# Performance work log

Measured on AMD Instinct MI355X. Metric: run time of the kernel, lower is better.

The kernel has to match this reference:

```python
import jax, jax.numpy as jnp
import numpy as np
import math

B, N, K, DV = 4, 8192, 32, 256
HID = 64


def _linear_params(key, n_in, n_out):
    # torch nn.Linear default init: U(-1/sqrt(n_in), 1/sqrt(n_in))
    kw, kb = jax.random.split(key)
    bound = 1.0 / math.sqrt(n_in)
    W = jax.random.uniform(kw, (n_out, n_in), jnp.float32, -bound, bound)
    b = jax.random.uniform(kb, (n_out,), jnp.float32, -bound, bound)
    return W, b


def setup_inputs() -> dict:
    key = jax.random.key(0)
    ks = jax.random.split(key, 9)
    q = jax.random.normal(ks[0], (B, N, 1, 3), jnp.float32)
    k = jax.random.normal(ks[1], (B, N, K, 3), jnp.float32)
    v = jax.random.normal(ks[2], (B, N, K, DV), jnp.float32)
    q_w0, q_b0 = _linear_params(ks[3], 3, HID)
    q_w1, q_b1 = _linear_params(ks[4], HID, HID)
    q_w2, q_b2 = _linear_params(ks[5], HID, HID)
    k_w0, k_b0 = _linear_params(ks[6], 3, HID)
    k_w1, k_b1 = _linear_params(ks[7], HID, HID)
    k_w2, k_b2 = _linear_params(ks[8], HID, HID)
    return {"q": q, "k": k, "v": v,
            "q_w0": q_w0, "q_b0": q_b0, "q_w1": q_w1, "q_b1": q_b1,
            "q_w2": q_w2, "q_b2": q_b2,
            "k_w0": k_w0, "k_b0": k_b0, "k_w1": k_w1, "k_b1": k_b1,
            "k_w2": k_w2, "k_b2": k_b2}


def _mlp(x, w0, b0, w1, b1, w2, b2):
    # 3-layer MLP: ReLU on first two layers, last layer linear
    x = jax.nn.relu(x @ w0.T + b0)
    x = jax.nn.relu(x @ w1.T + b1)
    return x @ w2.T + b2


def reference(q, k, v, q_w0, q_b0, q_w1, q_b1, q_w2, q_b2,
              k_w0, k_b0, k_w1, k_b1, k_w2, k_b2):
    # NOTE: scale uses the PRE-MLP last dim of q (=3), matching the torch code
    scale = 1.0 / math.sqrt(q.shape[-1])
    qe = _mlp(q, q_w0, q_b0, q_w1, q_b1, q_w2, q_b2)  # [B,N,1,64]
    ke = _mlp(k, k_w0, k_b0, k_w1, k_b1, k_w2, k_b2)  # [B,N,K,64]
    weight = jnp.einsum('bnqd,bnkd->bnqk', qe, ke) * scale  # [B,N,1,K]
    weight = jax.nn.softmax(weight, axis=-1)
    weight = jnp.squeeze(weight, -2)[..., None]             # [B,N,K,1]
    out = (weight * v).sum(-2)                              # [B,N,DV]
    return out
```

## Files before the change

kernel.cpp:

```cpp
#include <hip/hip_runtime.h>
#include <hip/hip_bf16.h>

typedef __attribute__((ext_vector_type(8))) short bf16x8;
typedef __attribute__((ext_vector_type(4))) float f32x4;

union BF8U { unsigned u[4]; bf16x8 v; };

#define PF 8

__device__ __forceinline__ unsigned f2bf1(float x){
  unsigned u = __builtin_bit_cast(unsigned, x);
  return (u + 0x7FFFu + ((u >> 16) & 1u)) >> 16;
}
__device__ __forceinline__ unsigned packbf(float a, float b){
  return f2bf1(a) | (f2bf1(b) << 16);
}
__device__ __forceinline__ unsigned cvt2(float a, float b){
  return (unsigned)__bfloat16_as_ushort(__float2bfloat16(a))
       | ((unsigned)__bfloat16_as_ushort(__float2bfloat16(b)) << 16);
}

__device__ __forceinline__ int act_addr(int r, int byteInRow){
  return r*128 + (byteInRow ^ ((r & 7) << 4));
}
#define LDS_SZ 16384

__global__ __launch_bounds__(256) void prep_kernel(
    const float* __restrict__ kw0, const float* __restrict__ kb0,
    const float* __restrict__ kw1, const float* __restrict__ kw2,
    const float* __restrict__ qw0, const float* __restrict__ qb0,
    const float* __restrict__ qw1, const float* __restrict__ qw2,
    unsigned* __restrict__ WF)
{
  const int t = threadIdx.x;
  const int path = blockIdx.x;
  const float* w0 = path ? qw0 : kw0;
  const float* b0 = path ? qb0 : kb0;
  const float* w1 = path ? qw1 : kw1;
  const float* w2 = path ? qw2 : kw2;
  unsigned* out = WF + path * 5120;
#pragma unroll
  for (int u = 0; u < 4; ++u) {
    int s2 = t + 256*u;
    int j2 = s2 & 3, l = (s2 >> 2) & 63, ct = s2 >> 8;
    int feat = 16*ct + (l & 15);
    int k0 = 8*(l >> 4) + 2*j2;
    float a = (k0   < 3) ? w0[feat*3 + k0]   : (k0   == 3 ? b0[feat] : 0.f);
    float b = (k0+1 < 3) ? w0[feat*3 + k0+1] : (k0+1 == 3 ? b0[feat] : 0.f);
    out[s2] = packbf(a, b);
  }
#pragma unroll
  for (int u = 0; u < 8; ++u) {
    int s2 = t + 256*u;
    int j2 = s2 & 3, l = (s2 >> 2) & 63, ctks = s2 >> 8;
    int feat = 16*(ctks & 3) + (l & 15);
    int k = 32*(ctks >> 2) + 8*(l >> 4) + 2*j2;
    out[1024 + s2] = packbf(w1[feat*64 + k], w1[feat*64 + k + 1]);
    out[3072 + s2] = packbf(w2[feat*64 + k], w2[feat*64 + k + 1]);
  }
}

__device__ __forceinline__ void mlp3(char* lds, int t,
    const float xv[2][3],
    const unsigned* __restrict__ WF,
    const float* __restrict__ b1, const float* __restrict__ b2,
    f32x4 acc2[4][2])
{
  const int lane = t & 63;
  const int q = lane >> 4, lm = lane & 15;
  const int wbase = (t >> 6) * 32;

  bf16x8 a0[2];
#pragma unroll
  for (int rt = 0; rt < 2; ++rt) {
    BF8U u;
    u.u[0] = (q == 0) ? cvt2(xv[rt][0], xv[rt][1]) : 0u;
    u.u[1] = (q == 0) ? cvt2(xv[rt][2], 1.0f)      : 0u;
    u.u[2] = 0u; u.u[3] = 0u;
    a0[rt] = u.v;
  }

  f32x4 h[4][2];

  {
    bf16x8 wf[4];
#pragma unroll
    for (int ft = 0; ft < 4; ++ft)
      wf[ft] = *(const bf16x8*)(WF + ft*256 + lane*4);
#pragma unroll
    for (int ft = 0; ft < 4; ++ft)
#pragma unroll
      for (int rt = 0; rt < 2; ++rt) {
        h[ft][rt] = (f32x4)(0.f);
        h[ft][rt] = __builtin_amdgcn_mfma_f32_16x16x32_bf16(wf[ft], a0[rt], h[ft][rt], 0, 0, 0);
      }
#pragma unroll
    for (int ft = 0; ft < 4; ++ft)
#pragma unroll
      for (int rt = 0; rt < 2; ++rt) {
        int rr = wbase + 16*rt + lm;
        f32x4 vv = h[ft][rt];
        uint2 wp;
        wp.x = cvt2(fmaxf(vv[0],0.f), fmaxf(vv[1],0.f));
        wp.y = cvt2(fmaxf(vv[2],0.f), fmaxf(vv[3],0.f));
        *(uint2*)(lds + act_addr(rr, (16*ft + 4*q)*2)) = wp;
      }
  }

  {
    bf16x8 a1[2][2];
#pragma unroll
    for (int rt = 0; rt < 2; ++rt)
#pragma unroll
      for (int ks = 0; ks < 2; ++ks)
        a1[rt][ks] = *(const bf16x8*)(lds + act_addr(wbase + 16*rt + lm, 64*ks + 16*q));
    bf16x8 wf[8];
#pragma unroll
    for (int c = 0; c < 8; ++c)
      wf[c] = *(const bf16x8*)(WF + 1024 + c*256 + lane*4);
#pragma unroll
    for (int ft = 0; ft < 4; ++ft)
#pragma unroll
      for (int rt = 0; rt < 2; ++rt) {
        h[ft][rt] = (f32x4)(0.f);
        h[ft][rt] = __builtin_amdgcn_mfma_f32_16x16x32_bf16(wf[ft],   a1[rt][0], h[ft][rt], 0, 0, 0);
        h[ft][rt] = __builtin_amdgcn_mfma_f32_16x16x32_bf16(wf[4+ft], a1[rt][1], h[ft][rt], 0, 0, 0);
      }
#pragma unroll
    for (int ft = 0; ft < 4; ++ft) {
      f32x4 b1f = *(const f32x4*)(b1 + 16*ft + 4*q);
#pragma unroll
      for (int rt = 0; rt < 2; ++rt) {
        int rr = wbase + 16*rt + lm;
        f32x4 vv = h[ft][rt];
        uint2 wp;
        wp.x = cvt2(fmaxf(vv[0]+b1f[0],0.f), fmaxf(vv[1]+b1f[1],0.f));
        wp.y = cvt2(fmaxf(vv[2]+b1f[2],0.f), fmaxf(vv[3]+b1f[3],0.f));
        *(uint2*)(lds + act_addr(rr, (16*ft + 4*q)*2)) = wp;
      }
    }
  }

  {
    bf16x8 a2[2][2];
#pragma unroll
    for (int rt = 0; rt < 2; ++rt)
#pragma unroll
      for (int ks = 0; ks < 2; ++ks)
        a2[rt][ks] = *(const bf16x8*)(lds + act_addr(wbase + 16*rt + lm, 64*ks + 16*q));
    bf16x8 wf[8];
#pragma unroll
    for (int c = 0; c < 8; ++c)
      wf[c] = *(const bf16x8*)(WF + 3072 + c*256 + lane*4);
#pragma unroll
    for (int ft = 0; ft < 4; ++ft)
#pragma unroll
      for (int rt = 0; rt < 2; ++rt) {
        acc2[ft][rt] = (f32x4)(0.f);
        acc2[ft][rt] = __builtin_amdgcn_mfma_f32_16x16x32_bf16(wf[ft],   a2[rt][0], acc2[ft][rt], 0, 0, 0);
        acc2[ft][rt] = __builtin_amdgcn_mfma_f32_16x16x32_bf16(wf[4+ft], a2[rt][1], acc2[ft][rt], 0, 0, 0);
      }
#pragma unroll
    for (int ft = 0; ft < 4; ++ft) {
      f32x4 b2f = *(const f32x4*)(b2 + 16*ft + 4*q);
#pragma unroll
      for (int rt = 0; rt < 2; ++rt)
#pragma unroll
        for (int i = 0; i < 4; ++i) acc2[ft][rt][i] += b2f[i];
    }
  }
}

__global__ __launch_bounds__(256, 3) void qe_mfma_kernel(
    const float* __restrict__ qin, const unsigned* __restrict__ WF,
    const float* __restrict__ b1, const float* __restrict__ b2,
    float* __restrict__ qeout)
{
  __shared__ __align__(16) char lds[LDS_SZ];
  const int t = threadIdx.x;
  const int lane = t & 63, wv = t >> 6, q = lane >> 4, lm = lane & 15;
  const long rowbase = (long)blockIdx.x * 128;
  const int wbase = wv * 32;
  float xv[2][3];
#pragma unroll
  for (int rt = 0; rt < 2; ++rt) {
    const float* xr = qin + (rowbase + wbase + 16*rt + lm) * 3;
    xv[rt][0] = xr[0]; xv[rt][1] = xr[1]; xv[rt][2] = xr[2];
  }
  f32x4 acc2[4][2];
  mlp3(lds, t, xv, WF, b1, b2, acc2);
#pragma unroll
  for (int ft = 0; ft < 4; ++ft)
#pragma unroll
    for (int rt = 0; rt < 2; ++rt) {
      long grow = rowbase + wbase + 16*rt + lm;
      *(f32x4*)(qeout + grow*64 + 16*ft + 4*q) = acc2[ft][rt];
    }
}

__global__ __launch_bounds__(256, 3) void attn_mfma_kernel(
    const float* __restrict__ kin, const float* __restrict__ v,
    const unsigned* __restrict__ WF,
    const float* __restrict__ b1, const float* __restrict__ b2,
    const float* __restrict__ qe, float* __restrict__ out)
{
  __shared__ __align__(16) char lds[LDS_SZ];
  const int t = threadIdx.x;
  const int lane = t & 63, wv = t >> 6, q = lane >> 4, lm = lane & 15;
  const long rowbase = (long)blockIdx.x * 128;
  const int wbase = wv * 32;
  const long G = (long)blockIdx.x * 4 + wv;

  float xv[2][3];
#pragma unroll
  for (int rt = 0; rt < 2; ++rt) {
    const float* xr = kin + (rowbase + wbase + 16*rt + lm) * 3;
    xv[rt][0] = xr[0]; xv[rt][1] = xr[1]; xv[rt][2] = xr[2];
  }
  __builtin_amdgcn_sched_barrier(0);

  const f32x4* vp = (const f32x4*)(v + G * 8192) + lane;
  f32x4 pre[PF];
#pragma unroll
  for (int s = 0; s < PF; ++s) pre[s] = vp[s * 64];
  __builtin_amdgcn_sched_barrier(0);

  f32x4 acc2[4][2];
  mlp3(lds, t, xv, WF, b1, b2, acc2);

  const float* qp = qe + G * 64;
  float p[2];
#pragma unroll
  for (int rt = 0; rt < 2; ++rt) {
    float s = 0.f;
#pragma unroll
    for (int ft = 0; ft < 4; ++ft) {
      f32x4 qv = *(const f32x4*)(qp + 16*ft + 4*q);
#pragma unroll
      for (int i = 0; i < 4; ++i) s += acc2[ft][rt][i] * qv[i];
    }
    s += __shfl_xor(s, 16, 64);
    s += __shfl_xor(s, 32, 64);
    p[rt] = s * 0.5773502691896258f;
  }

  float m = fmaxf(p[0], p[1]);
#pragma unroll
  for (int off = 1; off < 16; off <<= 1) m = fmaxf(m, __shfl_xor(m, off, 64));
  float e0 = __expf(p[0] - m), e1 = __expf(p[1] - m);
  float s = e0 + e1;
#pragma unroll
  for (int off = 1; off < 16; off <<= 1) s += __shfl_xor(s, off, 64);
  const float inv = 1.0f / s;
  float wgt[2] = { e0 * inv, e1 * inv };

  f32x4 acc = (f32x4)(0.f);
#pragma unroll
  for (int s2 = 0; s2 < PF; ++s2) {
    float wk = __shfl(wgt[s2 >> 4], s2 & 15, 64);
    acc += wk * pre[s2];
  }
#pragma unroll
  for (int k = PF; k < 32; ++k) {
    float wk = __shfl(wgt[k >> 4], k & 15, 64);
    f32x4 vv = vp[k * 64];
    acc += wk * vv;
  }
  *(f32x4*)(out + G * 256 + 4*lane) = acc;
}

extern "C" void kernel_launch(void* const* d_in, const int* in_sizes, int n_in,
                              void* d_out, int out_size, void* d_ws, size_t ws_size,
                              hipStream_t stream)
{
  const float* q   = (const float*)d_in[0];
  const float* k   = (const float*)d_in[1];
  const float* v   = (const float*)d_in[2];
  const float* qw0 = (const float*)d_in[3];
  const float* qb0 = (const float*)d_in[4];
  const float* qw1 = (const float*)d_in[5];
  const float* qb1 = (const float*)d_in[6];
  const float* qw2 = (const float*)d_in[7];
  const float* qb2 = (const float*)d_in[8];
  const float* kw0 = (const float*)d_in[9];
  const float* kb0 = (const float*)d_in[10];
  const float* kw1 = (const float*)d_in[11];
  const float* kb1 = (const float*)d_in[12];
  const float* kw2 = (const float*)d_in[13];
  const float* kb2 = (const float*)d_in[14];

  float*    qe = (float*)d_ws;
  unsigned* WF = (unsigned*)((char*)d_ws + (8u << 20));

  prep_kernel<<<2, 256, 0, stream>>>(kw0, kb0, kw1, kw2, qw0, qb0, qw1, qw2, WF);
  qe_mfma_kernel<<<256, 256, 0, stream>>>(q, WF + 5120, qb1, qb2, qe);
  attn_mfma_kernel<<<8192, 256, 0, stream>>>(k, v, WF, kb1, kb2, qe, (float*)d_out);
}
```

Measured before the change: 221.7 us.

## Prefetch first V rows into LDS via direct global-to-LDS loads

```diff
diff --git a/kernel.cpp b/kernel.cpp
--- a/kernel.cpp
+++ b/kernel.cpp
@@ -6,7 +6,8 @@
 
 union BF8U { unsigned u[4]; bf16x8 v; };
 
-#define PF 8
+#define PF_LDS 8
+#define PF_REG 8
 
 __device__ __forceinline__ unsigned f2bf1(float x){
   unsigned u = __builtin_bit_cast(unsigned, x);
@@ -23,7 +24,9 @@
 __device__ __forceinline__ int act_addr(int r, int byteInRow){
   return r*128 + (byteInRow ^ ((r & 7) << 4));
 }
-#define LDS_SZ 16384
+#define LDS_ACT 16384
+#define LDS_V   (LDS_ACT)
+#define LDS_SZ  (LDS_ACT + 4*PF_LDS*1024)
 
 __global__ __launch_bounds__(256) void prep_kernel(
     const float* __restrict__ kw0, const float* __restrict__ kb0,
@@ -176,7 +179,7 @@
     const float* __restrict__ b1, const float* __restrict__ b2,
     float* __restrict__ qeout)
 {
-  __shared__ __align__(16) char lds[LDS_SZ];
+  __shared__ __align__(16) char lds[LDS_ACT];
   const int t = threadIdx.x;
   const int lane = t & 63, wv = t >> 6, q = lane >> 4, lm = lane & 15;
   const long rowbase = (long)blockIdx.x * 128;
@@ -217,28 +220,39 @@
     const float* xr = kin + (rowbase + wbase + 16*rt + lm) * 3;
     xv[rt][0] = xr[0]; xv[rt][1] = xr[1]; xv[rt][2] = xr[2];
   }
+
+  const float* qp = qe + G * 64;
+  f32x4 qv[4];
+#pragma unroll
+  for (int ft = 0; ft < 4; ++ft) qv[ft] = *(const f32x4*)(qp + 16*ft + 4*q);
   __builtin_amdgcn_sched_barrier(0);
 
+  const char* gv = (const char*)(v + G * 8192);
+  char* vlds = lds + LDS_V + wv * (PF_LDS * 1024);
+#pragma unroll
+  for (int s = 0; s < PF_LDS; ++s)
+    __builtin_amdgcn_global_load_lds(
+        (const __attribute__((address_space(1))) void*)(gv + s*1024 + lane*16),
+        (__attribute__((address_space(3))) void*)(vlds + s*1024),
+        16, 0, 0);
   const f32x4* vp = (const f32x4*)(v + G * 8192) + lane;
-  f32x4 pre[PF];
-#pragma unroll
-  for (int s = 0; s < PF; ++s) pre[s] = vp[s * 64];
+  f32x4 pre[PF_REG];
+#pragma unroll
+  for (int s = 0; s < PF_REG; ++s)
+    pre[s] = __builtin_nontemporal_load(vp + (PF_LDS + s) * 64);
   __builtin_amdgcn_sched_barrier(0);
 
   f32x4 acc2[4][2];
   mlp3(lds, t, xv, WF, b1, b2, acc2);
 
-  const float* qp = qe + G * 64;
   float p[2];
 #pragma unroll
   for (int rt = 0; rt < 2; ++rt) {
     float s = 0.f;
 #pragma unroll
-    for (int ft = 0; ft < 4; ++ft) {
-      f32x4 qv = *(const f32x4*)(qp + 16*ft + 4*q);
-#pragma unroll
-      for (int i = 0; i < 4; ++i) s += acc2[ft][rt][i] * qv[i];
-    }
+    for (int ft = 0; ft < 4; ++ft)
+#pragma unroll
+      for (int i = 0; i < 4; ++i) s += acc2[ft][rt][i] * qv[ft][i];
     s += __shfl_xor(s, 16, 64);
     s += __shfl_xor(s, 32, 64);
     p[rt] = s * 0.5773502691896258f;
@@ -255,18 +269,26 @@
   float wgt[2] = { e0 * inv, e1 * inv };
 
   f32x4 acc = (f32x4)(0.f);
-#pragma unroll
-  for (int s2 = 0; s2 < PF; ++s2) {
-    float wk = __shfl(wgt[s2 >> 4], s2 & 15, 64);
+  asm volatile("s_waitcnt vmcnt(0)" ::: "memory");
+#pragma unroll
+  for (int s2 = 0; s2 < PF_LDS; ++s2) {
+    float wk = __shfl(wgt[0], s2, 64);
+    f32x4 vv = *(const f32x4*)(vlds + s2*1024 + lane*16);
+    acc += wk * vv;
+  }
+#pragma unroll
+  for (int s2 = 0; s2 < PF_REG; ++s2) {
+    int k = PF_LDS + s2;
+    float wk = __shfl(wgt[k >> 4], k & 15, 64);
     acc += wk * pre[s2];
   }
 #pragma unroll
-  for (int k = PF; k < 32; ++k) {
+  for (int k = PF_LDS + PF_REG; k < 32; ++k) {
     float wk = __shfl(wgt[k >> 4], k & 15, 64);
-    f32x4 vv = vp[k * 64];
+    f32x4 vv = __builtin_nontemporal_load(vp + k * 64);
     acc += wk * vv;
   }
-  *(f32x4*)(out + G * 256 + 4*lane) = acc;
+  __builtin_nontemporal_store(acc, (f32x4*)(out + G * 256 + 4*lane));
 }
 
 extern "C" void kernel_launch(void* const* d_in, const int* in_sizes, int n_in,
```

After: 190.6 us. 1.16x faster.
